# Optimization experiments

Hardware: AMD Instinct MI355X
Metric: run time of the kernel (lower is better)

The kernel has to match this reference:

```python
import jax, jax.numpy as jnp
import numpy as np

N, DIM, K = 131072, 64, 1024


def setup_inputs() -> dict:
    key = jax.random.key(0)
    kx, ke = jax.random.split(key)
    x = jax.random.normal(kx, (N, DIM), dtype=jnp.float32)
    # codebook buffer, initialized like uniform(-1/K, 1/K) in the original
    scale = 1.0 / K
    embedding = jax.random.uniform(ke, (K, DIM), dtype=jnp.float32, minval=-scale, maxval=scale)
    return {"x": x, "embedding": embedding}


def reference(x, embedding):
    # squared euclidean distances in fp32 (matches compute_distances)
    x32 = x.astype(jnp.float32)
    e32 = embedding.astype(jnp.float32)
    distances = (
        jnp.sum(x32 * x32, axis=1, keepdims=True)
        + jnp.sum(e32 * e32, axis=1)
        - 2.0 * jnp.einsum("nd,kd->nk", x32, e32)
    )
    indices = jnp.argmin(distances, axis=1)          # (N,)
    quantized = embedding[indices]                    # (N, DIM) codebook gather
    # commitment loss: mse(stop_grad(quantized), x)
    commitment_loss = jnp.mean((jax.lax.stop_gradient(quantized) - x) ** 2)
    # straight-through estimator
    quantized_st = x + jax.lax.stop_gradient(quantized - x)
    return quantized_st, indices, commitment_loss
```

## Files before the change

kernel.cpp:

```cpp
#include <hip/hip_runtime.h>
#include <hip/hip_bf16.h>

#define N_ROWS 131072
#define DIM 64
#define K_CODES 1024
#define NTILES 64
#define MARGIN 4e-5f
#define LIST_CAP 65536

typedef short short8 __attribute__((ext_vector_type(8)));
typedef float f32x4 __attribute__((ext_vector_type(4)));

__device__ __forceinline__ unsigned short f2bf(float f) {
    unsigned u = __float_as_uint(f);
    return (unsigned short)((u + 0x7fffu + ((u >> 16) & 1u)) >> 16);
}
__device__ __forceinline__ float bf2f(unsigned short h) {
    return __uint_as_float(((unsigned)h) << 16);
}
__device__ __forceinline__ unsigned med3u(unsigned a, unsigned b, unsigned c) {
    unsigned d;
    asm("v_med3_u32 %0, %1, %2, %3" : "=v"(d) : "v"(a), "v"(b), "v"(c));
    return d;
}
__device__ __forceinline__ unsigned minu(unsigned a, unsigned b) { return a < b ? a : b; }
__device__ __forceinline__ unsigned maxu(unsigned a, unsigned b) { return a > b ? a : b; }

__device__ __forceinline__ unsigned f2key(float v) {
    unsigned u = __float_as_uint(v);
    return u ^ (unsigned)(((int)u >> 31) | 0x80000000);
}
__device__ __forceinline__ float key2f(unsigned k) {
    unsigned kc = k & 0xFFFFFC00u;
    unsigned u = (kc & 0x80000000u) ? (kc ^ 0x80000000u) : ~kc;
    return __uint_as_float(u);
}

__device__ __forceinline__ float np_sq64(const float* __restrict__ v) {
    float xx[DIM];
    #pragma unroll
    for (int d = 0; d < DIM; ++d) xx[d] = v[d] * v[d];
    float r[8];
    #pragma unroll
    for (int j = 0; j < 8; ++j) r[j] = xx[j];
    #pragma unroll
    for (int i = 8; i < DIM; i += 8)
        #pragma unroll
        for (int j = 0; j < 8; ++j) r[j] = r[j] + xx[i + j];
    return ((r[0]+r[1]) + (r[2]+r[3])) + ((r[4]+r[5]) + (r[6]+r[7]));
}

__device__ __forceinline__ float np_dot64(const float* __restrict__ xv,
                                          const float* __restrict__ ek) {
    float a0 = 0.f, a1 = 0.f, a2 = 0.f, a3 = 0.f;
    #pragma unroll
    for (int c = 0; c < DIM; c += 16)
        #pragma unroll
        for (int b = 12; b >= 0; b -= 4) {
            const int d = c + b;
            a0 = a0 + xv[d+0] * ek[d+0];
            a1 = a1 + xv[d+1] * ek[d+1];
            a2 = a2 + xv[d+2] * ek[d+2];
            a3 = a3 + xv[d+3] * ek[d+3];
        }
    return (a0 + a1) + (a2 + a3);
}


__global__ void vq_prep(const float* __restrict__ emb, float* __restrict__ esq,
                        unsigned short* __restrict__ wsB,
                        unsigned int* __restrict__ cnt, float* __restrict__ loss) {
#pragma clang fp contract(off)
    const int t = blockIdx.x * blockDim.x + threadIdx.x;
    if (t == 0) { *cnt = 0u; *loss = 0.f; }
    const int k = t >> 2, c = t & 3;
    if (k >= K_CODES) return;
    const float* e = emb + (size_t)k * DIM;

    if (c == 0) esq[k] = np_sq64(e);

    const int off = (c & 1) * 32, sel = c >> 1;
    unsigned short val[32];
    #pragma unroll
    for (int j = 0; j < 32; ++j) {
        float v = e[off + j];
        unsigned short h = f2bf(v);
        val[j] = sel ? f2bf(v - bf2f(h)) : h;
    }
    const int tile = k >> 4, n = k & 15;
    #pragma unroll
    for (int g = 0; g < 4; ++g) {
        short8 s;
        #pragma unroll
        for (int j = 0; j < 8; ++j) s[j] = (short)val[g*8 + j];
        *reinterpret_cast<short8*>(wsB + ((size_t)((tile*4 + c)*64 + g*16 + n)) * 8) = s;
    }
}

__global__ __launch_bounds__(256, 2) void vq_mfma(const float* __restrict__ x,
        const float* __restrict__ emb, const float* __restrict__ esq,
        const unsigned short* __restrict__ wsB, float* __restrict__ out,
        unsigned int* __restrict__ cnt, unsigned int* __restrict__ list,
        float* __restrict__ loss) {
#pragma clang fp contract(off)
    const int tid = threadIdx.x;
    const int lane = tid & 63;
    const int w = tid >> 6;
    const int g = lane >> 4, res = lane & 15;
    const int rowbase = blockIdx.x * 256 + w * 64;

    short8 Ah[4][2], Al[4][2];
    #pragma unroll
    for (int rg = 0; rg < 4; ++rg) {
        const float* xr = x + (size_t)(rowbase + rg*16 + res) * DIM;
        #pragma unroll
        for (int h = 0; h < 2; ++h) {
            float4 v0 = *reinterpret_cast<const float4*>(xr + h*32 + g*8);
            float4 v1 = *reinterpret_cast<const float4*>(xr + h*32 + g*8 + 4);
            float xv[8] = {v0.x, v0.y, v0.z, v0.w, v1.x, v1.y, v1.z, v1.w};
            short8 sh, sl;
            #pragma unroll
            for (int j = 0; j < 8; ++j) {
                unsigned short hb = f2bf(xv[j]);
                sh[j] = (short)hb;
                sl[j] = (short)f2bf(xv[j] - bf2f(hb));
            }
            Ah[rg][h] = sh; Al[rg][h] = sl;
        }
    }

    unsigned b1[16], b2[16], b3[16];
    #pragma unroll
    for (int s = 0; s < 16; ++s) { b1[s] = 0xFFFFFFFFu; b2[s] = 0xFFFFFFFFu; b3[s] = 0xFFFFFFFFu; }

    auto loadB = [&](short8* Bd, int ct) {
        const unsigned short* bp = wsB + ((size_t)(ct*4)*64 + lane) * 8;
        #pragma unroll
        for (int c = 0; c < 4; ++c)
            Bd[c] = *reinterpret_cast<const short8*>(bp + (size_t)c * 64 * 8);
    };

    auto compute = [&](int ct, const short8* B, float esqv) {
        const unsigned kcur = (unsigned)(ct*16 + res);
        f32x4 acc[4];
        #pragma unroll
        for (int rg = 0; rg < 4; ++rg) acc[rg] = f32x4{0.f, 0.f, 0.f, 0.f};
        #pragma unroll
        for (int rg = 0; rg < 4; ++rg)
            acc[rg] = __builtin_amdgcn_mfma_f32_16x16x32_bf16(Ah[rg][0], B[0], acc[rg], 0,0,0);
        #pragma unroll
        for (int rg = 0; rg < 4; ++rg)
            acc[rg] = __builtin_amdgcn_mfma_f32_16x16x32_bf16(Ah[rg][1], B[1], acc[rg], 0,0,0);
        #pragma unroll
        for (int rg = 0; rg < 4; ++rg)
            acc[rg] = __builtin_amdgcn_mfma_f32_16x16x32_bf16(Ah[rg][0], B[2], acc[rg], 0,0,0);
        #pragma unroll
        for (int rg = 0; rg < 4; ++rg)
            acc[rg] = __builtin_amdgcn_mfma_f32_16x16x32_bf16(Ah[rg][1], B[3], acc[rg], 0,0,0);
        #pragma unroll
        for (int rg = 0; rg < 4; ++rg)
            acc[rg] = __builtin_amdgcn_mfma_f32_16x16x32_bf16(Al[rg][0], B[0], acc[rg], 0,0,0);
        #pragma unroll
        for (int rg = 0; rg < 4; ++rg)
            acc[rg] = __builtin_amdgcn_mfma_f32_16x16x32_bf16(Al[rg][1], B[1], acc[rg], 0,0,0);
        #pragma unroll
        for (int rg = 0; rg < 4; ++rg) {
            #pragma unroll
            for (int r = 0; r < 4; ++r) {
                float v = fmaf(-2.0f, acc[rg][r], esqv);
                unsigned key = (f2key(v) & 0xFFFFFC00u) | kcur;
                const int s = rg*4 + r;
                unsigned o1 = b1[s], o2 = b2[s];
                b3[s] = med3u(key, o2, b3[s]);
                b2[s] = med3u(key, o1, o2);
                b1[s] = minu(o1, key);
            }
        }
    };

    short8 BA[4], BB[4];
    loadB(BA, 0);
    for (int ct = 0; ct < NTILES; ct += 2) {
        float esqA = esq[ct*16 + res];
        float esqB = esq[(ct + 1)*16 + res];
        loadB(BB, ct + 1);
        compute(ct, BA, esqA);
        loadB(BA, (ct + 2) & 63);
        compute(ct + 1, BB, esqB);
    }

    #pragma unroll
    for (int m = 1; m < 16; m <<= 1) {
        #pragma unroll
        for (int s = 0; s < 16; ++s) {
            unsigned oa1 = __shfl_xor((int)b1[s], m, 64);
            unsigned oa2 = __shfl_xor((int)b2[s], m, 64);
            unsigned oa3 = __shfl_xor((int)b3[s], m, 64);
            unsigned m1 = minu(b1[s], oa1);
            unsigned m2 = minu(maxu(b1[s], oa1), minu(b2[s], oa2));
            unsigned m3 = minu(minu(maxu(b1[s], oa2), maxu(b2[s], oa1)),
                               minu(b3[s], oa3));
            b1[s] = m1; b2[s] = m2; b3[s] = m3;
        }
    }

    __shared__ unsigned s_k1[256], s_k2[256], s_k3[256];
    __shared__ int s_idx[256];
    if (res == 0) {
        #pragma unroll
        for (int s = 0; s < 16; ++s) {
            const int rl = w*64 + (s >> 2)*16 + g*4 + (s & 3);
            s_k1[rl] = b1[s]; s_k2[rl] = b2[s]; s_k3[rl] = b3[s];
        }
    }
    __syncthreads();

    {
        const int row = blockIdx.x * 256 + tid;
        unsigned k1 = s_k1[tid], k2 = s_k2[tid], k3 = s_k3[tid];
        float f1 = key2f(k1), f2 = key2f(k2), f3 = key2f(k3);
        int idx;
        if (f3 - f1 < MARGIN) {
            unsigned slot = atomicAdd(cnt, 1u);
            if (slot < LIST_CAP) list[slot] = (unsigned)row;
            idx = -1;
        } else if (f2 - f1 < MARGIN) {
            const int ia = (int)(k1 & 0x3FFu), ib = (int)(k2 & 0x3FFu);
            float xv[DIM];
            const float4* xp = reinterpret_cast<const float4*>(x + (size_t)row * DIM);
            #pragma unroll
            for (int q = 0; q < 16; ++q) {
                float4 v = xp[q];
                xv[4*q+0] = v.x; xv[4*q+1] = v.y; xv[4*q+2] = v.z; xv[4*q+3] = v.w;
            }
            float xsq = np_sq64(xv);
            float ta = xsq + esq[ia];
            float da = ta - 2.0f * np_dot64(xv, emb + (size_t)ia * DIM);
            float tb = xsq + esq[ib];
            float db = tb - 2.0f * np_dot64(xv, emb + (size_t)ib * DIM);
            idx = (da < db) ? ia : ((db < da) ? ib : (ia < ib ? ia : ib));
        } else {
            idx = (int)(k1 & 0x3FFu);
        }
        s_idx[tid] = idx;
    }
    __syncthreads();

    const int row = blockIdx.x * 256 + tid;
    const int idx = s_idx[tid];
    float lsum = 0.f;
    if (idx >= 0) {
        const float* xr = x + (size_t)row * DIM;
        const float* qr = emb + (size_t)idx * DIM;
        float* orow = out + (size_t)row * DIM;
        #pragma unroll
        for (int i = 0; i < 16; ++i) {
            float4 xv = reinterpret_cast<const float4*>(xr)[i];
            float4 qv = reinterpret_cast<const float4*>(qr)[i];
            float df0 = qv.x - xv.x, df1 = qv.y - xv.y;
            float df2 = qv.z - xv.z, df3 = qv.w - xv.w;
            lsum = fmaf(df0, df0, lsum); lsum = fmaf(df1, df1, lsum);
            lsum = fmaf(df2, df2, lsum); lsum = fmaf(df3, df3, lsum);
            float4 o = {xv.x + df0, xv.y + df1, xv.z + df2, xv.w + df3};
            reinterpret_cast<float4*>(orow)[i] = o;
        }
        out[(size_t)N_ROWS * DIM + row] = (float)idx;
    }
    #pragma unroll
    for (int off = 32; off > 0; off >>= 1) lsum += __shfl_down(lsum, off, 64);
    if (lane == 0) atomicAdd(loss, lsum);
}

__global__ void vq_fixup(const float* __restrict__ x, const float* __restrict__ emb,
                         const float* __restrict__ esq,
                         const unsigned int* __restrict__ cnt,
                         const unsigned int* __restrict__ list,
                         float* __restrict__ out, float* __restrict__ loss) {
#pragma clang fp contract(off)
    const int lane = threadIdx.x & 63;
    const int wid = (blockIdx.x * blockDim.x + threadIdx.x) >> 6;
    const int nw = (256 * 256) >> 6;
    unsigned count = *cnt;
    if (count > LIST_CAP) count = LIST_CAP;
    for (unsigned i = wid; i < count; i += nw) {
        const int row = (int)list[i];
        float xv[DIM];
        const float4* xp = reinterpret_cast<const float4*>(x + (size_t)row * DIM);
        #pragma unroll
        for (int q = 0; q < 16; ++q) {
            float4 v = xp[q];
            xv[4*q+0] = v.x; xv[4*q+1] = v.y; xv[4*q+2] = v.z; xv[4*q+3] = v.w;
        }
        float xsq = np_sq64(xv);
        float best = INFINITY; int bidx = 0x7fffffff;
        for (int t = 0; t < K_CODES / 64; ++t) {
            const int k = lane + t * 64;
            float dot = np_dot64(xv, emb + (size_t)k * DIM);
            float tt = xsq + esq[k];
            float dist = tt - 2.0f * dot;
            if (dist < best) { best = dist; bidx = k; }
        }
        #pragma unroll
        for (int m = 1; m < 64; m <<= 1) {
            float ob = __shfl_xor(best, m, 64);
            int   oi = __shfl_xor(bidx, m, 64);
            if (ob < best || (ob == best && oi < bidx)) { best = ob; bidx = oi; }
        }
        const float xd = x[(size_t)row * DIM + lane];
        const float qd = emb[(size_t)bidx * DIM + lane];
        const float df = qd - xd;
        out[(size_t)row * DIM + lane] = xd + df;
        if (lane == 0) out[(size_t)N_ROWS * DIM + row] = (float)bidx;
        float l2 = df * df;
        #pragma unroll
        for (int off = 32; off > 0; off >>= 1) l2 += __shfl_down(l2, off, 64);
        if (lane == 0) atomicAdd(loss, l2);
    }
}

__global__ void vq_final(const float* __restrict__ loss_acc, float* __restrict__ out_loss) {
    if (threadIdx.x == 0 && blockIdx.x == 0)
        out_loss[0] = loss_acc[0] / (float)((size_t)N_ROWS * DIM);
}

extern "C" void kernel_launch(void* const* d_in, const int* in_sizes, int n_in,
                              void* d_out, int out_size, void* d_ws, size_t ws_size,
                              hipStream_t stream) {
    const float* x   = (const float*)d_in[0];
    const float* emb = (const float*)d_in[1];
    float* out = (float*)d_out;

    unsigned int* cnt  = (unsigned int*)d_ws;
    float* loss        = (float*)d_ws + 1;
    float* esq         = (float*)d_ws + 4;
    unsigned short* wsB = (unsigned short*)((char*)d_ws + 8192);
    unsigned int* list = (unsigned int*)((char*)d_ws + 270336);

    vq_prep<<<dim3(16), dim3(256), 0, stream>>>(emb, esq, wsB, cnt, loss);
    vq_mfma<<<dim3(N_ROWS / 256), dim3(256), 0, stream>>>(x, emb, esq, wsB, out,
                                                          cnt, list, loss);
    vq_fixup<<<dim3(256), dim3(256), 0, stream>>>(x, emb, esq, cnt, list, out, loss);
    vq_final<<<dim3(1), dim3(1), 0, stream>>>(loss, out + (size_t)N_ROWS * DIM + N_ROWS);
}
```

Before: 144.7 us.

## Software-pipeline MFMA with top-3 key updates, use float med3 keys, split epilogue rows

The codebook loop now runs the MFMA block for the next tile before doing the top-3 key update for the previous tile, using two accumulator sets. The goal is to hide MFMA latency behind the VALU selection work. Keys are now built directly from raw float bits and ranked with fmed3/fmin, which removes the integer sign-flip transform. The output write now uses two threads per row, each handling half of the row, to improve coalescing. In exchange, accumulator register pressure goes up, and for negative distances the index bits packed into the key reverse the tie ordering. The existing near-tie margin checks are meant to cover that case.

```diff
diff --git a/kernel.cpp b/kernel.cpp
--- a/kernel.cpp
+++ b/kernel.cpp
@@ -17,23 +17,6 @@
 }
 __device__ __forceinline__ float bf2f(unsigned short h) {
     return __uint_as_float(((unsigned)h) << 16);
-}
-__device__ __forceinline__ unsigned med3u(unsigned a, unsigned b, unsigned c) {
-    unsigned d;
-    asm("v_med3_u32 %0, %1, %2, %3" : "=v"(d) : "v"(a), "v"(b), "v"(c));
-    return d;
-}
-__device__ __forceinline__ unsigned minu(unsigned a, unsigned b) { return a < b ? a : b; }
-__device__ __forceinline__ unsigned maxu(unsigned a, unsigned b) { return a > b ? a : b; }
-
-__device__ __forceinline__ unsigned f2key(float v) {
-    unsigned u = __float_as_uint(v);
-    return u ^ (unsigned)(((int)u >> 31) | 0x80000000);
-}
-__device__ __forceinline__ float key2f(unsigned k) {
-    unsigned kc = k & 0xFFFFFC00u;
-    unsigned u = (kc & 0x80000000u) ? (kc ^ 0x80000000u) : ~kc;
-    return __uint_as_float(u);
 }
 
 __device__ __forceinline__ float np_sq64(const float* __restrict__ v) {
@@ -129,9 +112,10 @@
         }
     }
 
-    unsigned b1[16], b2[16], b3[16];
-    #pragma unroll
-    for (int s = 0; s < 16; ++s) { b1[s] = 0xFFFFFFFFu; b2[s] = 0xFFFFFFFFu; b3[s] = 0xFFFFFFFFu; }
+    float b1[16], b2[16], b3[16];
+    const float FINF = __uint_as_float(0x7F800000u);
+    #pragma unroll
+    for (int s = 0; s < 16; ++s) { b1[s] = FINF; b2[s] = FINF; b3[s] = FINF; }
 
     auto loadB = [&](short8* Bd, int ct) {
         const unsigned short* bp = wsB + ((size_t)(ct*4)*64 + lane) * 8;
@@ -140,71 +124,83 @@
             Bd[c] = *reinterpret_cast<const short8*>(bp + (size_t)c * 64 * 8);
     };
 
-    auto compute = [&](int ct, const short8* B, float esqv) {
+    auto MF = [&](f32x4* acc, const short8* B) {
+        #pragma unroll
+        for (int rg = 0; rg < 4; ++rg) acc[rg] = f32x4{0.f, 0.f, 0.f, 0.f};
+        #pragma unroll
+        for (int rg = 0; rg < 4; ++rg)
+            acc[rg] = __builtin_amdgcn_mfma_f32_16x16x32_bf16(Ah[rg][0], B[0], acc[rg], 0,0,0);
+        #pragma unroll
+        for (int rg = 0; rg < 4; ++rg)
+            acc[rg] = __builtin_amdgcn_mfma_f32_16x16x32_bf16(Ah[rg][1], B[1], acc[rg], 0,0,0);
+        #pragma unroll
+        for (int rg = 0; rg < 4; ++rg)
+            acc[rg] = __builtin_amdgcn_mfma_f32_16x16x32_bf16(Ah[rg][0], B[2], acc[rg], 0,0,0);
+        #pragma unroll
+        for (int rg = 0; rg < 4; ++rg)
+            acc[rg] = __builtin_amdgcn_mfma_f32_16x16x32_bf16(Ah[rg][1], B[3], acc[rg], 0,0,0);
+        #pragma unroll
+        for (int rg = 0; rg < 4; ++rg)
+            acc[rg] = __builtin_amdgcn_mfma_f32_16x16x32_bf16(Al[rg][0], B[0], acc[rg], 0,0,0);
+        #pragma unroll
+        for (int rg = 0; rg < 4; ++rg)
+            acc[rg] = __builtin_amdgcn_mfma_f32_16x16x32_bf16(Al[rg][1], B[1], acc[rg], 0,0,0);
+    };
+
+    auto KY = [&](const f32x4* acc, float esqv, int ct) {
         const unsigned kcur = (unsigned)(ct*16 + res);
-        f32x4 acc[4];
-        #pragma unroll
-        for (int rg = 0; rg < 4; ++rg) acc[rg] = f32x4{0.f, 0.f, 0.f, 0.f};
-        #pragma unroll
-        for (int rg = 0; rg < 4; ++rg)
-            acc[rg] = __builtin_amdgcn_mfma_f32_16x16x32_bf16(Ah[rg][0], B[0], acc[rg], 0,0,0);
-        #pragma unroll
-        for (int rg = 0; rg < 4; ++rg)
-            acc[rg] = __builtin_amdgcn_mfma_f32_16x16x32_bf16(Ah[rg][1], B[1], acc[rg], 0,0,0);
-        #pragma unroll
-        for (int rg = 0; rg < 4; ++rg)
-            acc[rg] = __builtin_amdgcn_mfma_f32_16x16x32_bf16(Ah[rg][0], B[2], acc[rg], 0,0,0);
-        #pragma unroll
-        for (int rg = 0; rg < 4; ++rg)
-            acc[rg] = __builtin_amdgcn_mfma_f32_16x16x32_bf16(Ah[rg][1], B[3], acc[rg], 0,0,0);
-        #pragma unroll
-        for (int rg = 0; rg < 4; ++rg)
-            acc[rg] = __builtin_amdgcn_mfma_f32_16x16x32_bf16(Al[rg][0], B[0], acc[rg], 0,0,0);
-        #pragma unroll
-        for (int rg = 0; rg < 4; ++rg)
-            acc[rg] = __builtin_amdgcn_mfma_f32_16x16x32_bf16(Al[rg][1], B[1], acc[rg], 0,0,0);
         #pragma unroll
         for (int rg = 0; rg < 4; ++rg) {
             #pragma unroll
             for (int r = 0; r < 4; ++r) {
                 float v = fmaf(-2.0f, acc[rg][r], esqv);
-                unsigned key = (f2key(v) & 0xFFFFFC00u) | kcur;
+                float key = __uint_as_float((__float_as_uint(v) & 0xFFFFFC00u) | kcur);
                 const int s = rg*4 + r;
-                unsigned o1 = b1[s], o2 = b2[s];
-                b3[s] = med3u(key, o2, b3[s]);
-                b2[s] = med3u(key, o1, o2);
-                b1[s] = minu(o1, key);
+                float o1 = b1[s], o2 = b2[s];
+                b3[s] = __builtin_amdgcn_fmed3f(key, o2, b3[s]);
+                b2[s] = __builtin_amdgcn_fmed3f(key, o1, o2);
+                b1[s] = fminf(o1, key);
             }
         }
     };
 
-    short8 BA[4], BB[4];
-    loadB(BA, 0);
-    for (int ct = 0; ct < NTILES; ct += 2) {
-        float esqA = esq[ct*16 + res];
-        float esqB = esq[(ct + 1)*16 + res];
-        loadB(BB, ct + 1);
-        compute(ct, BA, esqA);
-        loadB(BA, (ct + 2) & 63);
-        compute(ct + 1, BB, esqB);
-    }
+    short8 B0[4], B1[4];
+    f32x4 accA[4], accB[4];
+    float e0, e1;
+
+    loadB(B0, 0); e0 = esq[res];
+    loadB(B1, 1); e1 = esq[16 + res];
+    MF(accA, B0);
+    for (int p = 0; p < 31; ++p) {
+        loadB(B0, 2*p + 2);
+        MF(accB, B1);
+        KY(accA, e0, 2*p);
+        e0 = esq[(2*p + 2)*16 + res];
+        loadB(B1, 2*p + 3);
+        MF(accA, B0);
+        KY(accB, e1, 2*p + 1);
+        e1 = esq[(2*p + 3)*16 + res];
+    }
+    MF(accB, B1);
+    KY(accA, e0, 62);
+    KY(accB, e1, 63);
 
     #pragma unroll
     for (int m = 1; m < 16; m <<= 1) {
         #pragma unroll
         for (int s = 0; s < 16; ++s) {
-            unsigned oa1 = __shfl_xor((int)b1[s], m, 64);
-            unsigned oa2 = __shfl_xor((int)b2[s], m, 64);
-            unsigned oa3 = __shfl_xor((int)b3[s], m, 64);
-            unsigned m1 = minu(b1[s], oa1);
-            unsigned m2 = minu(maxu(b1[s], oa1), minu(b2[s], oa2));
-            unsigned m3 = minu(minu(maxu(b1[s], oa2), maxu(b2[s], oa1)),
-                               minu(b3[s], oa3));
+            float oa1 = __shfl_xor(b1[s], m, 64);
+            float oa2 = __shfl_xor(b2[s], m, 64);
+            float oa3 = __shfl_xor(b3[s], m, 64);
+            float m1 = fminf(b1[s], oa1);
+            float m2 = fminf(fmaxf(b1[s], oa1), fminf(b2[s], oa2));
+            float m3 = fminf(fminf(fmaxf(b1[s], oa2), fmaxf(b2[s], oa1)),
+                             fminf(b3[s], oa3));
             b1[s] = m1; b2[s] = m2; b3[s] = m3;
         }
     }
 
-    __shared__ unsigned s_k1[256], s_k2[256], s_k3[256];
+    __shared__ float s_k1[256], s_k2[256], s_k3[256];
     __shared__ int s_idx[256];
     if (res == 0) {
         #pragma unroll
@@ -217,15 +213,19 @@
 
     {
         const int row = blockIdx.x * 256 + tid;
-        unsigned k1 = s_k1[tid], k2 = s_k2[tid], k3 = s_k3[tid];
-        float f1 = key2f(k1), f2 = key2f(k2), f3 = key2f(k3);
+        unsigned u1 = __float_as_uint(s_k1[tid]);
+        unsigned u2 = __float_as_uint(s_k2[tid]);
+        unsigned u3 = __float_as_uint(s_k3[tid]);
+        float f1 = __uint_as_float(u1 & 0xFFFFFC00u);
+        float f2 = __uint_as_float(u2 & 0xFFFFFC00u);
+        float f3 = __uint_as_float(u3 & 0xFFFFFC00u);
         int idx;
         if (f3 - f1 < MARGIN) {
             unsigned slot = atomicAdd(cnt, 1u);
             if (slot < LIST_CAP) list[slot] = (unsigned)row;
             idx = -1;
         } else if (f2 - f1 < MARGIN) {
-            const int ia = (int)(k1 & 0x3FFu), ib = (int)(k2 & 0x3FFu);
+            const int ia = (int)(u1 & 0x3FFu), ib = (int)(u2 & 0x3FFu);
             float xv[DIM];
             const float4* xp = reinterpret_cast<const float4*>(x + (size_t)row * DIM);
             #pragma unroll
@@ -240,31 +240,35 @@
             float db = tb - 2.0f * np_dot64(xv, emb + (size_t)ib * DIM);
             idx = (da < db) ? ia : ((db < da) ? ib : (ia < ib ? ia : ib));
         } else {
-            idx = (int)(k1 & 0x3FFu);
+            idx = (int)(u1 & 0x3FFu);
         }
         s_idx[tid] = idx;
     }
     __syncthreads();
 
-    const int row = blockIdx.x * 256 + tid;
-    const int idx = s_idx[tid];
     float lsum = 0.f;
-    if (idx >= 0) {
-        const float* xr = x + (size_t)row * DIM;
-        const float* qr = emb + (size_t)idx * DIM;
-        float* orow = out + (size_t)row * DIM;
-        #pragma unroll
-        for (int i = 0; i < 16; ++i) {
-            float4 xv = reinterpret_cast<const float4*>(xr)[i];
-            float4 qv = reinterpret_cast<const float4*>(qr)[i];
-            float df0 = qv.x - xv.x, df1 = qv.y - xv.y;
-            float df2 = qv.z - xv.z, df3 = qv.w - xv.w;
-            lsum = fmaf(df0, df0, lsum); lsum = fmaf(df1, df1, lsum);
-            lsum = fmaf(df2, df2, lsum); lsum = fmaf(df3, df3, lsum);
-            float4 o = {xv.x + df0, xv.y + df1, xv.z + df2, xv.w + df3};
-            reinterpret_cast<float4*>(orow)[i] = o;
-        }
-        out[(size_t)N_ROWS * DIM + row] = (float)idx;
+    #pragma unroll
+    for (int pass = 0; pass < 2; ++pass) {
+        const int rl = (tid >> 1) + pass * 128, half = tid & 1;
+        const int row = blockIdx.x * 256 + rl;
+        const int idx = s_idx[rl];
+        if (idx >= 0) {
+            const float* xr = x + (size_t)row * DIM + half*32;
+            const float* qr = emb + (size_t)idx * DIM + half*32;
+            float* orow = out + (size_t)row * DIM + half*32;
+            #pragma unroll
+            for (int i = 0; i < 8; ++i) {
+                float4 xv = reinterpret_cast<const float4*>(xr)[i];
+                float4 qv = reinterpret_cast<const float4*>(qr)[i];
+                float df0 = qv.x - xv.x, df1 = qv.y - xv.y;
+                float df2 = qv.z - xv.z, df3 = qv.w - xv.w;
+                lsum = fmaf(df0, df0, lsum); lsum = fmaf(df1, df1, lsum);
+                lsum = fmaf(df2, df2, lsum); lsum = fmaf(df3, df3, lsum);
+                float4 o = {xv.x + df0, xv.y + df1, xv.z + df2, xv.w + df3};
+                reinterpret_cast<float4*>(orow)[i] = o;
+            }
+            if (half == 0) out[(size_t)N_ROWS * DIM + row] = (float)idx;
+        }
     }
     #pragma unroll
     for (int off = 32; off > 0; off >>= 1) lsum += __shfl_down(lsum, off, 64);
```

Result: faster. 134.5 us (-7.0%).
